# Kernel tuning notes

Measured on AMD Instinct MI355X. Metric: run time of the kernel, lower is better.

## Reference

```python
import jax, jax.numpy as jnp
import numpy as np

N = 50000      # num_nodes
E = 800000     # num_edges
F_IN = 128     # node_features
H = 128        # hidden_channels
EPS = 1e-5     # BatchNorm eps


def setup_inputs() -> dict:
    key = jax.random.key(0)
    ks = jax.random.split(key, 6)
    x = jax.random.normal(ks[0], (N, F_IN), dtype=jnp.float32)
    edge_index = jax.random.randint(ks[1], (2, E), 0, N, dtype=jnp.int64)
    s = 0.05
    return {
        "x": x,
        "edge_index": edge_index,
        "g_in": jnp.ones((F_IN,), jnp.float32),
        "be_in": jnp.zeros((F_IN,), jnp.float32),
        "w1": jax.random.normal(ks[2], (F_IN, 2 * H), jnp.float32) * s,
        "b1": jnp.zeros((2 * H,), jnp.float32),
        "g1": jnp.ones((2 * H,), jnp.float32),
        "be1": jnp.zeros((2 * H,), jnp.float32),
        "w2": jax.random.normal(ks[3], (2 * H, H), jnp.float32) * s,
        "b2": jnp.zeros((H,), jnp.float32),
        "g2": jnp.ones((H,), jnp.float32),
        "be2": jnp.zeros((H,), jnp.float32),
    }


def batchnorm(x, g, b):
    # training-mode BatchNorm1d: batch stats over the node dimension (biased var)
    m = jnp.mean(x, axis=0)
    v = jnp.var(x, axis=0)
    return (x - m) * jax.lax.rsqrt(v + EPS) * g + b


def gcn_conv(x, w, b, src, dst, deg_inv_sqrt):
    # PyG GCNConv: transform, then D^{-1/2}(A+I)D^{-1/2} aggregation, then bias
    h = x @ w                                   # [N, out]
    norm = deg_inv_sqrt[src] * deg_inv_sqrt[dst]  # [E+N]
    msg = h[src] * norm[:, None]                # gather + scale
    out = jax.ops.segment_sum(msg, dst, num_segments=N)  # scatter-add
    return out + b


def reference(x, edge_index, g_in, be_in, w1, b1, g1, be1, w2, b2, g2, be2):
    # add self-loops once
    loop = jnp.arange(N, dtype=edge_index.dtype)
    src = jnp.concatenate([edge_index[0], loop])
    dst = jnp.concatenate([edge_index[1], loop])
    deg = jax.ops.segment_sum(jnp.ones_like(src, dtype=x.dtype), dst, num_segments=N)
    deg_inv_sqrt = jnp.where(deg > 0, jax.lax.rsqrt(jnp.maximum(deg, 1.0)), 0.0)

    h = batchnorm(x, g_in, be_in)
    # layer 1: F_IN -> 2H (no residual: shapes differ); dropout is identity in eval
    h = jax.nn.relu(batchnorm(gcn_conv(h, w1, b1, src, dst, deg_inv_sqrt), g1, be1))
    # layer 2 (final): 2H -> H
    h = jax.nn.relu(batchnorm(gcn_conv(h, w2, b2, src, dst, deg_inv_sqrt), g2, be2))
    return h
```

## Files before the change

kernel.cpp:

```cpp
#include <hip/hip_runtime.h>
#include <hip/hip_bf16.h>

#define NN 50000
#define NE 800000
#define FIN 128
#define HC1 256
#define HC2 128
#define EPSV 1e-5f
#define NTILE 196
#define CAP 8448
#define FILLMAX (CAP - 3840)

typedef __attribute__((ext_vector_type(8))) short bf8;
typedef __attribute__((ext_vector_type(16))) float f32x16;

union BF8U { bf8 v; ushort u[8]; uint4 q; };

__device__ __forceinline__ float bf2f(ushort u) {
    union { uint i; float f; } c; c.i = ((uint)u) << 16; return c.f;
}
__device__ __forceinline__ float ulo(uint u) {
    union { uint i; float f; } c; c.i = u << 16; return c.f;
}
__device__ __forceinline__ float uhi(uint u) {
    union { uint i; float f; } c; c.i = u & 0xffff0000u; return c.f;
}
__device__ __forceinline__ ushort f2bf(float f) {
    return __builtin_bit_cast(ushort, __float2bfloat16(f));
}

__global__ void k_init(int* __restrict__ gcur, float* __restrict__ stats, uint* __restrict__ s0row) {
    int i = blockIdx.x * blockDim.x + threadIdx.x;
    if (i < 256) gcur[i] = 0;
    if (i < 1024) stats[i] = 0.0f;
    if (i < 64) s0row[i] = 0u;
}

#define BKB 784
#define SB 391
#define WB 128

__device__ __forceinline__ void wprep_body(const float* __restrict__ W, ushort* __restrict__ wp,
                                           int idx, int K, int NC) {
    int j = idx & 7;
    int lane = (idx >> 3) & 63;
    int ts = idx >> 9;
    int KS = K / 16;
    int s = ts % KS;
    int t = ts / KS;
    int n = t * 32 + (lane & 31);
    int k = s * 16 + (lane >> 5) * 8 + j;
    wp[idx] = f2bf(W[(size_t)k * NC + n]);
}

__global__ __launch_bounds__(256) void k_bucket(
    const int* __restrict__ ei, int* __restrict__ gcur, uint* __restrict__ buckets,
    const float* __restrict__ x, float* __restrict__ sum, float* __restrict__ sumsq,
    const float* __restrict__ w1, ushort* __restrict__ wp1,
    const float* __restrict__ w2, ushort* __restrict__ wp2) {
    int b = blockIdx.x;
    int t = threadIdx.x;
    if (b < BKB) {
        __shared__ int hist[NTILE];
        __shared__ int base[NTILE];
        if (t < NTILE) hist[t] = 0;
        __syncthreads();
        int e0 = b * 1024;
        int es[4], ed[4];
#pragma unroll
        for (int i = 0; i < 4; ++i) {
            int e = e0 + i * 256 + t;
            if (e < NE) {
                int s = ei[e];
                int d = ei[NE + e];
                s = min(max(s, 0), NN - 1);
                d = min(max(d, 0), NN - 1);
                es[i] = s; ed[i] = d;
                atomicAdd(&hist[d >> 8], 1);
            } else es[i] = -1;
        }
        __syncthreads();
        if (t < NTILE) base[t] = atomicAdd(&gcur[t], hist[t]);
        __syncthreads();
        if (t < NTILE) hist[t] = 0;
        __syncthreads();
#pragma unroll
        for (int i = 0; i < 4; ++i) {
            if (es[i] >= 0) {
                int tile = ed[i] >> 8;
                int lofs = atomicAdd(&hist[tile], 1);
                int pos = base[tile] + lofs;
                if (pos < CAP) buckets[(size_t)tile * CAP + pos] = ((uint)es[i] << 8) | (uint)(ed[i] & 255);
            }
        }
        return;
    }
    if (b < BKB + SB) {
        const int F4 = 32, RIF = 8, RPB = 128;
        int c4 = t & 31;
        int ro = t >> 5;
        int r0 = (b - BKB) * RPB;
        int r1 = min(r0 + RPB, NN);
        float4 s = make_float4(0.f, 0.f, 0.f, 0.f);
        float4 q = make_float4(0.f, 0.f, 0.f, 0.f);
        for (int r = r0 + ro; r < r1; r += RIF) {
            float4 v = ((const float4*)x)[(size_t)r * F4 + c4];
            s.x += v.x; s.y += v.y; s.z += v.z; s.w += v.w;
            q.x += v.x * v.x; q.y += v.y * v.y; q.z += v.z * v.z; q.w += v.w * v.w;
        }
        __shared__ float4 sS[256];
        __shared__ float4 sQ[256];
        sS[t] = s; sQ[t] = q;
        __syncthreads();
#pragma unroll
        for (int st = 128; st >= 32; st >>= 1) {
            if (t < st) {
                float4 a = sS[t + st], bb = sQ[t + st];
                sS[t].x += a.x; sS[t].y += a.y; sS[t].z += a.z; sS[t].w += a.w;
                sQ[t].x += bb.x; sQ[t].y += bb.y; sQ[t].z += bb.z; sQ[t].w += bb.w;
            }
            __syncthreads();
        }
        if (t < 32) {
            float4 a = sS[t], bb = sQ[t];
            atomicAdd(&sum[t * 4 + 0], a.x); atomicAdd(&sum[t * 4 + 1], a.y);
            atomicAdd(&sum[t * 4 + 2], a.z); atomicAdd(&sum[t * 4 + 3], a.w);
            atomicAdd(&sumsq[t * 4 + 0], bb.x); atomicAdd(&sumsq[t * 4 + 1], bb.y);
            atomicAdd(&sumsq[t * 4 + 2], bb.z); atomicAdd(&sumsq[t * 4 + 3], bb.w);
        }
        return;
    }
    if (b < BKB + SB + WB) {
        wprep_body(w1, wp1, (b - BKB - SB) * 256 + t, FIN, HC1);
        return;
    }
    wprep_body(w2, wp2, (b - BKB - SB - WB) * 256 + t, HC1, HC2);
}

__global__ __launch_bounds__(256) void k_csr(
    const int* __restrict__ gcur, const uint* __restrict__ buckets,
    ushort* __restrict__ csr, int* __restrict__ cnt, int* __restrict__ rowstart,
    const float* __restrict__ sum, const float* __restrict__ sumsq,
    const float* __restrict__ g, const float* __restrict__ be,
    float* __restrict__ scale, float* __restrict__ shift) {
    int t = threadIdx.x;
    if (blockIdx.x == NTILE) {
        if (t < 128) {
            float mean = sum[t] / (float)NN;
            float var = sumsq[t] / (float)NN - mean * mean;
            var = fmaxf(var, 0.f);
            float sc = g[t] * rsqrtf(var + EPSV);
            scale[t] = sc;
            shift[t] = be[t] - mean * sc;
        }
        return;
    }
    __shared__ uint ubuf[CAP];
    __shared__ int cnt256[256];
    __shared__ int scan[256];
    __shared__ int offs256[256];
    __shared__ int cur256[256];
    int tile = blockIdx.x;
    int t0 = tile << 8;
    int size = min(gcur[tile], FILLMAX);
    cnt256[t] = 0;
    __syncthreads();
    for (int i = t; i < size; i += 256) {
        uint u = buckets[(size_t)tile * CAP + i];
        ubuf[i] = u;
        atomicAdd(&cnt256[u & 255u], 1);
    }
    __syncthreads();
    int c = cnt256[t];
    int padded = (c + 15) & ~15;
    scan[t] = padded;
    __syncthreads();
#pragma unroll
    for (int off = 1; off < 256; off <<= 1) {
        int v = (t >= off) ? scan[t - off] : 0;
        __syncthreads();
        scan[t] += v;
        __syncthreads();
    }
    int excl = scan[t] - padded;
    offs256[t] = excl;
    cur256[t] = 0;
    int r = t0 + t;
    if (r < NN) {
        cnt[r] = c;
        rowstart[r] = tile * CAP + excl;
    }
    __syncthreads();
    for (int i = t; i < size; i += 256) {
        uint u = ubuf[i];
        int l = u & 255u;
        int p = atomicAdd(&cur256[l], 1);
        int w = offs256[l] + p;
        if (w < CAP) csr[(size_t)tile * CAP + w] = (ushort)(u >> 8);
    }
    if (r < NN) {
        for (int p = c; p < padded; ++p) {
            int w = excl + p;
            if (w < CAP) csr[(size_t)tile * CAP + w] = (ushort)NN;
        }
    }
}

__global__ void k_s0(const float* __restrict__ x, const int* __restrict__ cnt,
                     const float* __restrict__ scale, const float* __restrict__ shift,
                     ushort* __restrict__ s0) {
    int idx = blockIdx.x * blockDim.x + threadIdx.x;
    const int total = NN * FIN / 4;
    if (idx >= total) return;
    int row = idx >> 5;
    int c4 = idx & 31;
    float4 v = ((const float4*)x)[idx];
    float4 sc = ((const float4*)scale)[c4];
    float4 sh = ((const float4*)shift)[c4];
    float d = rsqrtf((float)(cnt[row] + 1));
    ushort4 o;
    o.x = f2bf((v.x * sc.x + sh.x) * d);
    o.y = f2bf((v.y * sc.y + sh.y) * d);
    o.z = f2bf((v.z * sc.z + sh.z) * d);
    o.w = f2bf((v.w * sc.w + sh.w) * d);
    ((ushort4*)s0)[idx] = o;
}

__global__ __launch_bounds__(256) void k_gather(
    const int* __restrict__ cnt, const int* __restrict__ rowstart,
    const ushort* __restrict__ csr, const ushort* __restrict__ src,
    ushort* __restrict__ agg) {
    int wid = threadIdx.x >> 6;
    int lane = threadIdx.x & 63;
    int r = blockIdx.x * 4 + wid;
    if (r >= NN) return;
    int deg = cnt[r];
    int padded = (deg + 15) & ~15;
    int base = rowstart[r];
    const uint* sp = (const uint*)src;
    uint v = sp[(size_t)r * 64 + lane];
    float a0 = ulo(v), a1 = uhi(v);
    for (int j = 0; j < padded; j += 16) {
        const ushort* p = csr + base + j;
        uint4 q0 = *(const uint4*)p;
        uint4 q1 = *(const uint4*)(p + 8);
        uint id[16];
        id[0]  = q0.x & 0xffffu; id[1]  = q0.x >> 16;
        id[2]  = q0.y & 0xffffu; id[3]  = q0.y >> 16;
        id[4]  = q0.z & 0xffffu; id[5]  = q0.z >> 16;
        id[6]  = q0.w & 0xffffu; id[7]  = q0.w >> 16;
        id[8]  = q1.x & 0xffffu; id[9]  = q1.x >> 16;
        id[10] = q1.y & 0xffffu; id[11] = q1.y >> 16;
        id[12] = q1.z & 0xffffu; id[13] = q1.z >> 16;
        id[14] = q1.w & 0xffffu; id[15] = q1.w >> 16;
#pragma unroll
        for (int k = 0; k < 16; ++k) id[k] = min(id[k], (uint)NN);
        uint vv[16];
#pragma unroll
        for (int k = 0; k < 16; ++k) vv[k] = sp[(size_t)id[k] * 64 + lane];
#pragma unroll
        for (int k = 0; k < 16; ++k) { a0 += ulo(vv[k]); a1 += uhi(vv[k]); }
    }
    float d = rsqrtf((float)(deg + 1));
    uint o = ((uint)f2bf(a1 * d) << 16) | (uint)f2bf(a0 * d);
    ((uint*)agg)[(size_t)r * 64 + lane] = o;
}

__global__ __launch_bounds__(256) void k_mm1(
    const ushort* __restrict__ Abf,
    const ushort* __restrict__ wp,
    const float* __restrict__ bias,
    ushort* __restrict__ Y,
    float* __restrict__ sum, float* __restrict__ sumsq)
{
    const int K = 128, NC = 256, KS = K / 16, NT = NC / 32;
    int tid = threadIdx.x;
    int wid = tid >> 6;
    int lane = tid & 63;
    int rbase = blockIdx.x * 128 + wid * 32;
    int arow = rbase + (lane & 31);
    int khalf = lane >> 5;

    __shared__ float lsum[NC];
    __shared__ float lsq[NC];
    lsum[tid] = 0.f; lsq[tid] = 0.f;
    __syncthreads();

    f32x16 acc[NT];
#pragma unroll
    for (int t = 0; t < NT; ++t)
#pragma unroll
        for (int i = 0; i < 16; ++i) acc[t][i] = 0.f;

    const uint4* Bq = (const uint4*)wp;
    const uint4* Aq = (const uint4*)Abf;
#pragma unroll
    for (int s = 0; s < KS; ++s) {
        BF8U au;
        if (arow < NN) au.q = Aq[(size_t)arow * (K / 8) + s * 2 + khalf];
        else au.q = make_uint4(0, 0, 0, 0);
#pragma unroll
        for (int t = 0; t < NT; ++t) {
            BF8U bu;
            bu.q = Bq[(t * KS + s) * 64 + lane];
            acc[t] = __builtin_amdgcn_mfma_f32_32x32x16_bf16(au.v, bu.v, acc[t], 0, 0, 0);
        }
    }

#pragma unroll
    for (int t = 0; t < NT; ++t) {
        int col = t * 32 + (lane & 31);
        float bv = bias[col];
        float fs = 0.f, fq = 0.f;
#pragma unroll
        for (int q = 0; q < 4; ++q) {
#pragma unroll
            for (int i = 0; i < 4; ++i) {
                int r = rbase + q * 8 + khalf * 4 + i;
                if (r < NN) {
                    float v = acc[t][q * 4 + i] + bv;
                    Y[(size_t)r * NC + col] = f2bf(v);
                    fs += v; fq += v * v;
                }
            }
        }
        atomicAdd(&lsum[col], fs);
        atomicAdd(&lsq[col], fq);
    }
    __syncthreads();
    atomicAdd(&sum[tid], lsum[tid]);
    atomicAdd(&sumsq[tid], lsq[tid]);
}

__global__ __launch_bounds__(256) void k_mm2(
    const ushort* __restrict__ Y,
    const ushort* __restrict__ wp,
    const float* __restrict__ sum1, const float* __restrict__ sq1,
    const float* __restrict__ g1, const float* __restrict__ be1,
    const int* __restrict__ cnt,
    ushort* __restrict__ S2)
{
    const int K = 256, NC = 128, KS = K / 16, NT = NC / 32;
    __shared__ float ssc[K];
    __shared__ float ssh[K];
    {
        int c = threadIdx.x;
        float mean = sum1[c] / (float)NN;
        float var = fmaxf(sq1[c] / (float)NN - mean * mean, 0.f);
        float s = g1[c] * rsqrtf(var + EPSV);
        ssc[c] = s;
        ssh[c] = be1[c] - mean * s;
    }
    __syncthreads();

    int wid = threadIdx.x >> 6;
    int lane = threadIdx.x & 63;
    int rbase = blockIdx.x * 128 + wid * 32;
    int arow = rbase + (lane & 31);
    int khalf = lane >> 5;

    f32x16 acc[NT];
#pragma unroll
    for (int t = 0; t < NT; ++t)
#pragma unroll
        for (int i = 0; i < 16; ++i) acc[t][i] = 0.f;

    const uint4* Bq = (const uint4*)wp;
#pragma unroll
    for (int s = 0; s < KS; ++s) {
        int k0 = s * 16 + khalf * 8;
        BF8U au;
        if (arow < NN) {
            uint4 y = *(const uint4*)&Y[(size_t)arow * K + k0];
            float4 c0 = *(const float4*)&ssc[k0];
            float4 c1 = *(const float4*)&ssc[k0 + 4];
            float4 h0 = *(const float4*)&ssh[k0];
            float4 h1 = *(const float4*)&ssh[k0 + 4];
            au.u[0] = f2bf(fmaxf(bf2f((ushort)(y.x & 0xffffu)) * c0.x + h0.x, 0.f));
            au.u[1] = f2bf(fmaxf(bf2f((ushort)(y.x >> 16))     * c0.y + h0.y, 0.f));
            au.u[2] = f2bf(fmaxf(bf2f((ushort)(y.y & 0xffffu)) * c0.z + h0.z, 0.f));
            au.u[3] = f2bf(fmaxf(bf2f((ushort)(y.y >> 16))     * c0.w + h0.w, 0.f));
            au.u[4] = f2bf(fmaxf(bf2f((ushort)(y.z & 0xffffu)) * c1.x + h1.x, 0.f));
            au.u[5] = f2bf(fmaxf(bf2f((ushort)(y.z >> 16))     * c1.y + h1.y, 0.f));
            au.u[6] = f2bf(fmaxf(bf2f((ushort)(y.w & 0xffffu)) * c1.z + h1.z, 0.f));
            au.u[7] = f2bf(fmaxf(bf2f((ushort)(y.w >> 16))     * c1.w + h1.w, 0.f));
        } else {
            au.q = make_uint4(0, 0, 0, 0);
        }
#pragma unroll
        for (int t = 0; t < NT; ++t) {
            BF8U bu;
            bu.q = Bq[(t * KS + s) * 64 + lane];
            acc[t] = __builtin_amdgcn_mfma_f32_32x32x16_bf16(au.v, bu.v, acc[t], 0, 0, 0);
        }
    }

#pragma unroll
    for (int q = 0; q < 4; ++q) {
#pragma unroll
        for (int i = 0; i < 4; ++i) {
            int r = rbase + q * 8 + khalf * 4 + i;
            if (r < NN) {
                float dv = rsqrtf((float)(cnt[r] + 1));
#pragma unroll
                for (int t = 0; t < NT; ++t) {
                    int col = t * 32 + (lane & 31);
                    S2[(size_t)r * NC + col] = f2bf(acc[t][q * 4 + i] * dv);
                }
            }
        }
    }
}

__global__ __launch_bounds__(256) void k_post2(const ushort* __restrict__ agg2,
                                               const float* __restrict__ b2,
                                               float* __restrict__ sum, float* __restrict__ sumsq) {
    const int F4 = 32, RIF = 8, RPB = 128;
    int t = threadIdx.x;
    int c4 = t & 31;
    int ro = t >> 5;
    int r0 = blockIdx.x * RPB;
    int r1 = min(r0 + RPB, NN);
    float4 bb = ((const float4*)b2)[c4];
    float4 s = make_float4(0.f, 0.f, 0.f, 0.f);
    float4 q = make_float4(0.f, 0.f, 0.f, 0.f);
    for (int r = r0 + ro; r < r1; r += RIF) {
        ushort4 u = ((const ushort4*)agg2)[(size_t)r * F4 + c4];
        float4 v;
        v.x = bf2f(u.x) + bb.x; v.y = bf2f(u.y) + bb.y;
        v.z = bf2f(u.z) + bb.z; v.w = bf2f(u.w) + bb.w;
        s.x += v.x; s.y += v.y; s.z += v.z; s.w += v.w;
        q.x += v.x * v.x; q.y += v.y * v.y; q.z += v.z * v.z; q.w += v.w * v.w;
    }
    __shared__ float4 sS[256];
    __shared__ float4 sQ[256];
    sS[t] = s; sQ[t] = q;
    __syncthreads();
#pragma unroll
    for (int st = 128; st >= F4; st >>= 1) {
        if (t < st) {
            float4 a = sS[t + st], b = sQ[t + st];
            sS[t].x += a.x; sS[t].y += a.y; sS[t].z += a.z; sS[t].w += a.w;
            sQ[t].x += b.x; sQ[t].y += b.y; sQ[t].z += b.z; sQ[t].w += b.w;
        }
        __syncthreads();
    }
    if (t < F4) {
        float4 a = sS[t], b = sQ[t];
        atomicAdd(&sum[t * 4 + 0], a.x); atomicAdd(&sum[t * 4 + 1], a.y);
        atomicAdd(&sum[t * 4 + 2], a.z); atomicAdd(&sum[t * 4 + 3], a.w);
        atomicAdd(&sumsq[t * 4 + 0], b.x); atomicAdd(&sumsq[t * 4 + 1], b.y);
        atomicAdd(&sumsq[t * 4 + 2], b.z); atomicAdd(&sumsq[t * 4 + 3], b.w);
    }
}

__global__ void k_bnrelu(const ushort* __restrict__ agg2, const float* __restrict__ b2,
                         const float* __restrict__ sum, const float* __restrict__ sumsq,
                         const float* __restrict__ g, const float* __restrict__ be,
                         float* __restrict__ out) {
    int idx = blockIdx.x * blockDim.x + threadIdx.x;
    const int total = NN * HC2 / 4;
    if (idx >= total) return;
    int c4 = idx & 31;
    float4 sm = ((const float4*)sum)[c4];
    float4 sq = ((const float4*)sumsq)[c4];
    float4 gg = ((const float4*)g)[c4];
    float4 bee = ((const float4*)be)[c4];
    float4 bb = ((const float4*)b2)[c4];
    float4 mean, sc, sh;
    mean.x = sm.x / (float)NN; mean.y = sm.y / (float)NN;
    mean.z = sm.z / (float)NN; mean.w = sm.w / (float)NN;
    sc.x = gg.x * rsqrtf(fmaxf(sq.x / (float)NN - mean.x * mean.x, 0.f) + EPSV);
    sc.y = gg.y * rsqrtf(fmaxf(sq.y / (float)NN - mean.y * mean.y, 0.f) + EPSV);
    sc.z = gg.z * rsqrtf(fmaxf(sq.z / (float)NN - mean.z * mean.z, 0.f) + EPSV);
    sc.w = gg.w * rsqrtf(fmaxf(sq.w / (float)NN - mean.w * mean.w, 0.f) + EPSV);
    sh.x = bee.x - mean.x * sc.x; sh.y = bee.y - mean.y * sc.y;
    sh.z = bee.z - mean.z * sc.z; sh.w = bee.w - mean.w * sc.w;
    ushort4 u = ((const ushort4*)agg2)[idx];
    float4 v;
    v.x = fmaxf((bf2f(u.x) + bb.x) * sc.x + sh.x, 0.f);
    v.y = fmaxf((bf2f(u.y) + bb.y) * sc.y + sh.y, 0.f);
    v.z = fmaxf((bf2f(u.z) + bb.z) * sc.z + sh.z, 0.f);
    v.w = fmaxf((bf2f(u.w) + bb.w) * sc.w + sh.w, 0.f);
    ((float4*)out)[idx] = v;
}

extern "C" void kernel_launch(void* const* d_in, const int* in_sizes, int n_in,
                              void* d_out, int out_size, void* d_ws, size_t ws_size,
                              hipStream_t stream) {
    const float* x     = (const float*)d_in[0];
    const int*   ei    = (const int*)d_in[1];
    const float* g_in  = (const float*)d_in[2];
    const float* be_in = (const float*)d_in[3];
    const float* w1    = (const float*)d_in[4];
    const float* b1    = (const float*)d_in[5];
    const float* g1    = (const float*)d_in[6];
    const float* be1   = (const float*)d_in[7];
    const float* w2    = (const float*)d_in[8];
    const float* b2    = (const float*)d_in[9];
    const float* g2    = (const float*)d_in[10];
    const float* be2   = (const float*)d_in[11];
    float* out = (float*)d_out;

    float* ws = (float*)d_ws;
    float* stats = ws;
    float* sumIn = stats;        float* sqIn = stats + 128;
    float* sum1  = stats + 256;  float* sq1  = stats + 512;
    float* sum2  = stats + 768;  float* sq2  = stats + 896;
    float* params = ws + 1024;
    float* scIn = params;        float* shIn = params + 128;
    ushort* wp1   = (ushort*)(ws + 2048);
    ushort* wp2   = (ushort*)(ws + 18432);
    ushort* y1u   = (ushort*)(ws + 34816);
    ushort* s0bf  = (ushort*)(ws + 6434816);
    ushort* aggbf = (ushort*)(ws + 9634880);
    int* cnt      = (int*)(ws + 12834880);
    int* rowstart = (int*)(ws + 12884880);
    int* gcur     = (int*)(ws + 12934880);
    uint* buckets = (uint*)(ws + 12935136);
    ushort* csr   = (ushort*)(ws + 14590944);

    const int sblocks = (NN + 127) / 128;

    hipLaunchKernelGGL(k_init, dim3(4), dim3(256), 0, stream,
                       gcur, stats, (uint*)s0bf + (size_t)NN * 64);

    hipLaunchKernelGGL(k_bucket, dim3(BKB + SB + 2 * WB), dim3(256), 0, stream,
                       ei, gcur, buckets, x, sumIn, sqIn, w1, wp1, w2, wp2);

    hipLaunchKernelGGL(k_csr, dim3(NTILE + 1), dim3(256), 0, stream,
                       gcur, buckets, csr, cnt, rowstart,
                       sumIn, sqIn, g_in, be_in, scIn, shIn);

    hipLaunchKernelGGL(k_s0, dim3((NN * 32 + 255) / 256), dim3(256), 0, stream,
                       x, cnt, scIn, shIn, s0bf);

    hipLaunchKernelGGL(k_gather, dim3((NN + 3) / 4), dim3(256), 0, stream,
                       cnt, rowstart, csr, s0bf, aggbf);

    hipLaunchKernelGGL(k_mm1, dim3(sblocks), dim3(256), 0, stream, aggbf, wp1, b1, y1u, sum1, sq1);

    hipLaunchKernelGGL(k_mm2, dim3(sblocks), dim3(256), 0, stream,
                       y1u, wp2, sum1, sq1, g1, be1, cnt, s0bf);
    hipLaunchKernelGGL(k_gather, dim3((NN + 3) / 4), dim3(256), 0, stream,
                       cnt, rowstart, csr, s0bf, aggbf);

    hipLaunchKernelGGL(k_post2, dim3(sblocks), dim3(256), 0, stream, aggbf, b2, sum2, sq2);
    hipLaunchKernelGGL(k_bnrelu, dim3((NN * 32 + 255) / 256), dim3(256), 0, stream,
                       aggbf, b2, sum2, sq2, g2, be2, out);
}
```

Before: 255.7 us.

## Fuse input BN into CSR build, fold layer-2 stats into gather, coarsen bucketing

The input BatchNorm scale/shift computation and the normalized bf16 row write move into the CSR kernel, which removes the separate k_s0 launch. The second gather becomes a grid-stride kernel with 784 blocks that also accumulates the layer-2 BatchNorm sums, replacing the k_post2 pass over the aggregated tensor. The bucketing kernel now processes 4096 edges per block with fewer blocks, which cuts global atomics on the tile cursors but gives less parallelism. The grid-stride gather with 784 blocks may hide latency worse than the fully parallel version.

```diff
diff --git a/kernel.cpp b/kernel.cpp
--- a/kernel.cpp
+++ b/kernel.cpp
@@ -10,6 +10,7 @@
 #define NTILE 196
 #define CAP 8448
 #define FILLMAX (CAP - 3840)
+#define NQ 12500
 
 typedef __attribute__((ext_vector_type(8))) short bf8;
 typedef __attribute__((ext_vector_type(16))) float f32x16;
@@ -36,7 +37,7 @@
     if (i < 64) s0row[i] = 0u;
 }
 
-#define BKB 784
+#define BKB NTILE
 #define SB 391
 #define WB 128
 
@@ -65,10 +66,10 @@
         __shared__ int base[NTILE];
         if (t < NTILE) hist[t] = 0;
         __syncthreads();
-        int e0 = b * 1024;
-        int es[4], ed[4];
-#pragma unroll
-        for (int i = 0; i < 4; ++i) {
+        int e0 = b * 4096;
+        int es[16], ed[16];
+#pragma unroll
+        for (int i = 0; i < 16; ++i) {
             int e = e0 + i * 256 + t;
             if (e < NE) {
                 int s = ei[e];
@@ -85,7 +86,7 @@
         if (t < NTILE) hist[t] = 0;
         __syncthreads();
 #pragma unroll
-        for (int i = 0; i < 4; ++i) {
+        for (int i = 0; i < 16; ++i) {
             if (es[i] >= 0) {
                 int tile = ed[i] >> 8;
                 int lofs = atomicAdd(&hist[tile], 1);
@@ -140,28 +141,27 @@
 __global__ __launch_bounds__(256) void k_csr(
     const int* __restrict__ gcur, const uint* __restrict__ buckets,
     ushort* __restrict__ csr, int* __restrict__ cnt, int* __restrict__ rowstart,
-    const float* __restrict__ sum, const float* __restrict__ sumsq,
+    const float* __restrict__ sumIn, const float* __restrict__ sqIn,
     const float* __restrict__ g, const float* __restrict__ be,
-    float* __restrict__ scale, float* __restrict__ shift) {
-    int t = threadIdx.x;
-    if (blockIdx.x == NTILE) {
-        if (t < 128) {
-            float mean = sum[t] / (float)NN;
-            float var = sumsq[t] / (float)NN - mean * mean;
-            var = fmaxf(var, 0.f);
-            float sc = g[t] * rsqrtf(var + EPSV);
-            scale[t] = sc;
-            shift[t] = be[t] - mean * sc;
-        }
-        return;
-    }
+    const float* __restrict__ x, ushort* __restrict__ s0) {
     __shared__ uint ubuf[CAP];
     __shared__ int cnt256[256];
     __shared__ int scan[256];
     __shared__ int offs256[256];
     __shared__ int cur256[256];
+    __shared__ int dcnt[256];
+    __shared__ float ssc[128];
+    __shared__ float ssh[128];
+    int t = threadIdx.x;
     int tile = blockIdx.x;
     int t0 = tile << 8;
+    if (t < 128) {
+        float mean = sumIn[t] / (float)NN;
+        float var = fmaxf(sqIn[t] / (float)NN - mean * mean, 0.f);
+        float s = g[t] * rsqrtf(var + EPSV);
+        ssc[t] = s;
+        ssh[t] = be[t] - mean * s;
+    }
     int size = min(gcur[tile], FILLMAX);
     cnt256[t] = 0;
     __syncthreads();
@@ -172,6 +172,7 @@
     }
     __syncthreads();
     int c = cnt256[t];
+    dcnt[t] = c;
     int padded = (c + 15) & ~15;
     scan[t] = padded;
     __syncthreads();
@@ -204,66 +205,93 @@
             if (w < CAP) csr[(size_t)tile * CAP + w] = (ushort)NN;
         }
     }
-}
-
-__global__ void k_s0(const float* __restrict__ x, const int* __restrict__ cnt,
-                     const float* __restrict__ scale, const float* __restrict__ shift,
-                     ushort* __restrict__ s0) {
-    int idx = blockIdx.x * blockDim.x + threadIdx.x;
-    const int total = NN * FIN / 4;
-    if (idx >= total) return;
-    int row = idx >> 5;
-    int c4 = idx & 31;
-    float4 v = ((const float4*)x)[idx];
-    float4 sc = ((const float4*)scale)[c4];
-    float4 sh = ((const float4*)shift)[c4];
-    float d = rsqrtf((float)(cnt[row] + 1));
-    ushort4 o;
-    o.x = f2bf((v.x * sc.x + sh.x) * d);
-    o.y = f2bf((v.y * sc.y + sh.y) * d);
-    o.z = f2bf((v.z * sc.z + sh.z) * d);
-    o.w = f2bf((v.w * sc.w + sh.w) * d);
-    ((ushort4*)s0)[idx] = o;
-}
-
+    {
+        int c4 = t & 31;
+        float4 sc = *(const float4*)&ssc[c4 * 4];
+        float4 sh = *(const float4*)&ssh[c4 * 4];
+        for (int rr = t >> 5; rr < 256; rr += 8) {
+            int row = t0 + rr;
+            if (row >= NN) break;
+            float d = rsqrtf((float)(dcnt[rr] + 1));
+            float4 v = ((const float4*)x)[(size_t)row * 32 + c4];
+            ushort4 o;
+            o.x = f2bf((v.x * sc.x + sh.x) * d);
+            o.y = f2bf((v.y * sc.y + sh.y) * d);
+            o.z = f2bf((v.z * sc.z + sh.z) * d);
+            o.w = f2bf((v.w * sc.w + sh.w) * d);
+            ((ushort4*)s0)[(size_t)row * 32 + c4] = o;
+        }
+    }
+}
+
+template<int STATS>
 __global__ __launch_bounds__(256) void k_gather(
     const int* __restrict__ cnt, const int* __restrict__ rowstart,
     const ushort* __restrict__ csr, const ushort* __restrict__ src,
-    ushort* __restrict__ agg) {
-    int wid = threadIdx.x >> 6;
-    int lane = threadIdx.x & 63;
-    int r = blockIdx.x * 4 + wid;
-    if (r >= NN) return;
-    int deg = cnt[r];
-    int padded = (deg + 15) & ~15;
-    int base = rowstart[r];
+    ushort* __restrict__ agg, const float* __restrict__ b2,
+    float* __restrict__ sum, float* __restrict__ sumsq) {
+    __shared__ float lsum[128];
+    __shared__ float lsq[128];
+    int tid = threadIdx.x;
+    int wid = tid >> 6;
+    int lane = tid & 63;
+    float bb0 = 0.f, bb1 = 0.f, fs0 = 0.f, fq0 = 0.f, fs1 = 0.f, fq1 = 0.f;
+    if (STATS) {
+        if (tid < 128) { lsum[tid] = 0.f; lsq[tid] = 0.f; }
+        bb0 = b2[2 * lane];
+        bb1 = b2[2 * lane + 1];
+        __syncthreads();
+    }
     const uint* sp = (const uint*)src;
-    uint v = sp[(size_t)r * 64 + lane];
-    float a0 = ulo(v), a1 = uhi(v);
-    for (int j = 0; j < padded; j += 16) {
-        const ushort* p = csr + base + j;
-        uint4 q0 = *(const uint4*)p;
-        uint4 q1 = *(const uint4*)(p + 8);
-        uint id[16];
-        id[0]  = q0.x & 0xffffu; id[1]  = q0.x >> 16;
-        id[2]  = q0.y & 0xffffu; id[3]  = q0.y >> 16;
-        id[4]  = q0.z & 0xffffu; id[5]  = q0.z >> 16;
-        id[6]  = q0.w & 0xffffu; id[7]  = q0.w >> 16;
-        id[8]  = q1.x & 0xffffu; id[9]  = q1.x >> 16;
-        id[10] = q1.y & 0xffffu; id[11] = q1.y >> 16;
-        id[12] = q1.z & 0xffffu; id[13] = q1.z >> 16;
-        id[14] = q1.w & 0xffffu; id[15] = q1.w >> 16;
-#pragma unroll
-        for (int k = 0; k < 16; ++k) id[k] = min(id[k], (uint)NN);
-        uint vv[16];
-#pragma unroll
-        for (int k = 0; k < 16; ++k) vv[k] = sp[(size_t)id[k] * 64 + lane];
-#pragma unroll
-        for (int k = 0; k < 16; ++k) { a0 += ulo(vv[k]); a1 += uhi(vv[k]); }
-    }
-    float d = rsqrtf((float)(deg + 1));
-    uint o = ((uint)f2bf(a1 * d) << 16) | (uint)f2bf(a0 * d);
-    ((uint*)agg)[(size_t)r * 64 + lane] = o;
+    for (int q = blockIdx.x; q < NQ; q += gridDim.x) {
+        int r = q * 4 + wid;
+        int deg = cnt[r];
+        int padded = (deg + 15) & ~15;
+        int base = rowstart[r];
+        uint v = sp[(size_t)r * 64 + lane];
+        float a0 = ulo(v), a1 = uhi(v);
+        for (int j = 0; j < padded; j += 16) {
+            const ushort* p = csr + base + j;
+            uint4 q0 = *(const uint4*)p;
+            uint4 q1 = *(const uint4*)(p + 8);
+            uint id[16];
+            id[0]  = q0.x & 0xffffu; id[1]  = q0.x >> 16;
+            id[2]  = q0.y & 0xffffu; id[3]  = q0.y >> 16;
+            id[4]  = q0.z & 0xffffu; id[5]  = q0.z >> 16;
+            id[6]  = q0.w & 0xffffu; id[7]  = q0.w >> 16;
+            id[8]  = q1.x & 0xffffu; id[9]  = q1.x >> 16;
+            id[10] = q1.y & 0xffffu; id[11] = q1.y >> 16;
+            id[12] = q1.z & 0xffffu; id[13] = q1.z >> 16;
+            id[14] = q1.w & 0xffffu; id[15] = q1.w >> 16;
+#pragma unroll
+            for (int k = 0; k < 16; ++k) id[k] = min(id[k], (uint)NN);
+            uint vv[16];
+#pragma unroll
+            for (int k = 0; k < 16; ++k) vv[k] = sp[(size_t)id[k] * 64 + lane];
+#pragma unroll
+            for (int k = 0; k < 16; ++k) { a0 += ulo(vv[k]); a1 += uhi(vv[k]); }
+        }
+        float d = rsqrtf((float)(deg + 1));
+        float a0f = a0 * d, a1f = a1 * d;
+        if (STATS) {
+            float v0 = a0f + bb0, v1 = a1f + bb1;
+            fs0 += v0; fq0 += v0 * v0;
+            fs1 += v1; fq1 += v1 * v1;
+        }
+        uint o = ((uint)f2bf(a1f) << 16) | (uint)f2bf(a0f);
+        ((uint*)agg)[(size_t)r * 64 + lane] = o;
+    }
+    if (STATS) {
+        atomicAdd(&lsum[2 * lane], fs0);
+        atomicAdd(&lsum[2 * lane + 1], fs1);
+        atomicAdd(&lsq[2 * lane], fq0);
+        atomicAdd(&lsq[2 * lane + 1], fq1);
+        __syncthreads();
+        if (tid < 128) {
+            atomicAdd(&sum[tid], lsum[tid]);
+            atomicAdd(&sumsq[tid], lsq[tid]);
+        }
+    }
 }
 
 __global__ __launch_bounds__(256) void k_mm1(
@@ -409,48 +437,6 @@
                 }
             }
         }
-    }
-}
-
-__global__ __launch_bounds__(256) void k_post2(const ushort* __restrict__ agg2,
-                                               const float* __restrict__ b2,
-                                               float* __restrict__ sum, float* __restrict__ sumsq) {
-    const int F4 = 32, RIF = 8, RPB = 128;
-    int t = threadIdx.x;
-    int c4 = t & 31;
-    int ro = t >> 5;
-    int r0 = blockIdx.x * RPB;
-    int r1 = min(r0 + RPB, NN);
-    float4 bb = ((const float4*)b2)[c4];
-    float4 s = make_float4(0.f, 0.f, 0.f, 0.f);
-    float4 q = make_float4(0.f, 0.f, 0.f, 0.f);
-    for (int r = r0 + ro; r < r1; r += RIF) {
-        ushort4 u = ((const ushort4*)agg2)[(size_t)r * F4 + c4];
-        float4 v;
-        v.x = bf2f(u.x) + bb.x; v.y = bf2f(u.y) + bb.y;
-        v.z = bf2f(u.z) + bb.z; v.w = bf2f(u.w) + bb.w;
-        s.x += v.x; s.y += v.y; s.z += v.z; s.w += v.w;
-        q.x += v.x * v.x; q.y += v.y * v.y; q.z += v.z * v.z; q.w += v.w * v.w;
-    }
-    __shared__ float4 sS[256];
-    __shared__ float4 sQ[256];
-    sS[t] = s; sQ[t] = q;
-    __syncthreads();
-#pragma unroll
-    for (int st = 128; st >= F4; st >>= 1) {
-        if (t < st) {
-            float4 a = sS[t + st], b = sQ[t + st];
-            sS[t].x += a.x; sS[t].y += a.y; sS[t].z += a.z; sS[t].w += a.w;
-            sQ[t].x += b.x; sQ[t].y += b.y; sQ[t].z += b.z; sQ[t].w += b.w;
-        }
-        __syncthreads();
-    }
-    if (t < F4) {
-        float4 a = sS[t], b = sQ[t];
-        atomicAdd(&sum[t * 4 + 0], a.x); atomicAdd(&sum[t * 4 + 1], a.y);
-        atomicAdd(&sum[t * 4 + 2], a.z); atomicAdd(&sum[t * 4 + 3], a.w);
-        atomicAdd(&sumsq[t * 4 + 0], b.x); atomicAdd(&sumsq[t * 4 + 1], b.y);
-        atomicAdd(&sumsq[t * 4 + 2], b.z); atomicAdd(&sumsq[t * 4 + 3], b.w);
     }
 }
 
@@ -507,8 +493,6 @@
     float* sumIn = stats;        float* sqIn = stats + 128;
     float* sum1  = stats + 256;  float* sq1  = stats + 512;
     float* sum2  = stats + 768;  float* sq2  = stats + 896;
-    float* params = ws + 1024;
-    float* scIn = params;        float* shIn = params + 128;
     ushort* wp1   = (ushort*)(ws + 2048);
     ushort* wp2   = (ushort*)(ws + 18432);
     ushort* y1u   = (ushort*)(ws + 34816);
@@ -528,24 +512,21 @@
     hipLaunchKernelGGL(k_bucket, dim3(BKB + SB + 2 * WB), dim3(256), 0, stream,
                        ei, gcur, buckets, x, sumIn, sqIn, w1, wp1, w2, wp2);
 
-    hipLaunchKernelGGL(k_csr, dim3(NTILE + 1), dim3(256), 0, stream,
+    hipLaunchKernelGGL(k_csr, dim3(NTILE), dim3(256), 0, stream,
                        gcur, buckets, csr, cnt, rowstart,
-                       sumIn, sqIn, g_in, be_in, scIn, shIn);
-
-    hipLaunchKernelGGL(k_s0, dim3((NN * 32 + 255) / 256), dim3(256), 0, stream,
-                       x, cnt, scIn, shIn, s0bf);
-
-    hipLaunchKernelGGL(k_gather, dim3((NN + 3) / 4), dim3(256), 0, stream,
-                       cnt, rowstart, csr, s0bf, aggbf);
+                       sumIn, sqIn, g_in, be_in, x, s0bf);
+
+    hipLaunchKernelGGL(k_gather<0>, dim3(NQ), dim3(256), 0, stream,
+                       cnt, rowstart, csr, s0bf, aggbf, nullptr, nullptr, nullptr);
 
     hipLaunchKernelGGL(k_mm1, dim3(sblocks), dim3(256), 0, stream, aggbf, wp1, b1, y1u, sum1, sq1);
 
     hipLaunchKernelGGL(k_mm2, dim3(sblocks), dim3(256), 0, stream,
                        y1u, wp2, sum1, sq1, g1, be1, cnt, s0bf);
-    hipLaunchKernelGGL(k_gather, dim3((NN + 3) / 4), dim3(256), 0, stream,
-                       cnt, rowstart, csr, s0bf, aggbf);
-
-    hipLaunchKernelGGL(k_post2, dim3(sblocks), dim3(256), 0, stream, aggbf, b2, sum2, sq2);
+
+    hipLaunchKernelGGL(k_gather<1>, dim3(784), dim3(256), 0, stream,
+                       cnt, rowstart, csr, s0bf, aggbf, b2, sum2, sq2);
+
     hipLaunchKernelGGL(k_bnrelu, dim3((NN * 32 + 255) / 256), dim3(256), 0, stream,
                        aggbf, b2, sum2, sq2, g2, be2, out);
 }
```

Result: faster. 229.2 us (-10.4%).
